# Kernel tuning notes

Measured on AMD Instinct MI355X. Metric: run time of the kernel, lower is better.

## Reference

```python
import jax, jax.numpy as jnp
import numpy as np

B, U, S, F, D = 4, 1024, 256, 16, 256
K_RED = 3          # fd_redundancy_k
MAX_STEPS = 32     # fixed trip count replacing the data-dependent while-loop
NEG = -1e9


def setup_inputs() -> dict:
    key = jax.random.key(0)
    ks = jax.random.split(key, 12)
    user_enc = jax.random.normal(ks[0], (B, U, D), dtype=jnp.float32)
    server_enc = jax.random.normal(ks[1], (B, S, D), dtype=jnp.float32)
    # small needs vs. generous capacities so the allocation loop runs many steps
    users = jax.random.uniform(ks[2], (B, U, 8), dtype=jnp.float32) * 0.1
    servers = jax.random.uniform(ks[3], (B, S, 8), dtype=jnp.float32) * 20.0 + 1.0
    connect = jax.random.uniform(ks[4], (B, U, S)) < 0.3
    fd_id = jax.random.randint(ks[5], (B, S), 0, F)
    fd_onehot = jax.nn.one_hot(fd_id, F, dtype=jnp.float32)
    W_state = jax.random.normal(ks[6], (D, 4), dtype=jnp.float32) * 0.5
    b_state = jnp.zeros((D,), dtype=jnp.float32)
    W_q = jax.random.normal(ks[7], (D, D), dtype=jnp.float32) * D ** -0.5
    W_k = jax.random.normal(ks[8], (D, D), dtype=jnp.float32) * D ** -0.5
    W_us = jax.random.normal(ks[9], (1, 3), dtype=jnp.float32) * 0.5
    return dict(user_enc=user_enc, server_enc=server_enc, users=users, servers=servers,
                connect=connect, fd_onehot=fd_onehot, W_state=W_state, b_state=b_state,
                W_q=W_q, W_k=W_k, W_us=W_us,
                fd_alpha=jnp.asarray(1.0, jnp.float32), fd_beta=jnp.asarray(0.0, jnp.float32),
                score_bias=jnp.asarray(0.0, jnp.float32))


def _forward(user_enc, server_enc, users, servers, connect, fd_onehot,
             W_state, b_state, W_q, W_k, W_us, fd_alpha, fd_beta, score_bias):
    b, u, _ = users.shape
    s = servers.shape[1]
    d = user_enc.shape[-1]
    needs = users[..., 2:6]            # [B,U,4]
    init_cap = servers[..., 3:7]       # [B,S,4]
    inv_sqrt_d = d ** -0.5
    kf = jnp.asarray(float(K_RED), jnp.float32)
    q = user_enc @ W_q.T               # [B,U,D]
    u_ids = jnp.arange(u)[None, :, None]   # [1,U,1]
    s_ids = jnp.arange(s)[None, None, :]   # [1,1,S]
    b_grid = jnp.broadcast_to(jnp.arange(b)[:, None], (b, s))

    def step(carry, _):
        cap, alloc, fd_seen, logp = carry
        rc = jnp.sum(alloc, axis=-1)                                   # [B,U]
        need_more = rc < K_RED
        can_fulfill = jnp.all(cap[:, None] >= needs[:, :, None], -1)   # [B,U,S]
        elig = connect & can_fulfill & need_more[:, :, None] & (~alloc)
        elig = elig & jnp.any(elig)                                    # freeze when done
        # fault-domain novelty score
        fd_overlap = jnp.einsum('buf,bsf->bus', fd_seen, fd_onehot)
        is_new_fd = (fd_overlap < 0.5).astype(jnp.float32)
        # capacity-conditioned server keys
        cap_ratio = cap / jnp.maximum(init_cap, 1e-6)
        k_vec = (server_enc + cap_ratio @ W_state.T + b_state) @ W_k.T
        logits = jnp.einsum('bud,bsd->bus', q, k_vec) * inv_sqrt_d + score_bias
        logits = logits + jnp.tanh(fd_alpha * is_new_fd + fd_beta)
        rc_f = rc.astype(jnp.float32)
        user_state = jnp.stack([rc_f / kf, jnp.clip(kf - rc_f, 0.0) / kf,
                                (rc == K_RED - 1).astype(jnp.float32)], axis=-1)
        logits = logits + user_state @ W_us.T                          # [B,U,1] bcast
        cand = jnp.where(elig, logits, NEG)
        valid_server = jnp.any(elig, axis=1)                           # [B,S]
        # each valid server proposes its best user (greedy policy)
        prop_u = jnp.argmax(cand, axis=1)                              # [B,S]
        logp_bs = jnp.max(cand, axis=1) - jax.scipy.special.logsumexp(cand, axis=1)
        prop_mask = valid_server[:, None, :] & (prop_u[:, None, :] == u_ids)  # [B,U,S]
        # each proposed user accepts its best proposing server
        chosen_s = jnp.argmax(jnp.where(prop_mask, logits, NEG), axis=-1)     # [B,U]
        has_prop = jnp.any(prop_mask, axis=-1)
        sel = has_prop[..., None] & (s_ids == chosen_s[..., None])     # [B,U,S]
        alloc = alloc | sel
        fd_contrib = jnp.where(valid_server[..., None], fd_onehot, 0.0)
        fd_seen = fd_seen.at[b_grid, prop_u].max(fd_contrib)
        used = jnp.einsum('bus,buc->bsc', sel.astype(jnp.float32), needs)
        cap = jnp.maximum(cap - used, 0.0)
        logp = logp + jnp.sum(jnp.where(prop_mask, logp_bs[:, None, :], 0.0), axis=-1)
        return (cap, alloc, fd_seen, logp), None

    init = (init_cap,
            jnp.zeros((b, u, s), dtype=bool),
            jnp.zeros((b, u, fd_onehot.shape[-1]), dtype=jnp.float32),
            jnp.zeros((b, u), dtype=jnp.float32))
    (cap, alloc, fd_seen, logp), _ = jax.lax.scan(step, init, None, length=MAX_STEPS)
    return logp.sum(axis=1), alloc, cap


def reference(user_enc, server_enc, users, servers, connect, fd_onehot,
              W_state, b_state, W_q, W_k, W_us, fd_alpha, fd_beta, score_bias):
    return _forward(user_enc, server_enc, users, servers, connect, fd_onehot,
                    W_state, b_state, W_q, W_k, W_us, fd_alpha, fd_beta, score_bias)
```

## Files before the change

kernel.cpp:

```cpp
#include <hip/hip_runtime.h>
#include <stdint.h>
#include <math.h>

#define NB 4
#define NU 1024
#define NS 256
#define NF 16
#define ND 256
#define NEGV -1000000000.0f
#define VBIT (1u << 14)
#define AGENT __HIP_MEMORY_SCOPE_AGENT
#define SPINCAP (1 << 20)
#define NGRP 64
#define SPB 4
#define NT 1024


__device__ __forceinline__ void gemm64_body(
    const float* __restrict__ A, const float* __restrict__ Bm, float* __restrict__ C,
    int K, int lda, int ldb, int ldc, const float* __restrict__ biasA, float alpha,
    int m0, int n0, int t,
    float (&As)[2][16][68], float (&Bs)[2][16][68]) {
  int tx = t & 15, ty = t >> 4;
  float acc[4][4];
#pragma unroll
  for (int i = 0; i < 4; i++)
#pragma unroll
    for (int j = 0; j < 4; j++) acc[i][j] = 0.f;
  int lr = t >> 2;
  int kq = (t & 3) * 4;
  {
    float4 av = *(const float4*)(A + (size_t)(m0 + lr) * lda + kq);
    if (biasA) {
      const float* bp = biasA + kq;
      av.x += bp[0]; av.y += bp[1]; av.z += bp[2]; av.w += bp[3];
    }
    As[0][kq + 0][lr] = av.x; As[0][kq + 1][lr] = av.y;
    As[0][kq + 2][lr] = av.z; As[0][kq + 3][lr] = av.w;
    float4 bv = *(const float4*)(Bm + (size_t)(n0 + lr) * ldb + kq);
    Bs[0][kq + 0][lr] = bv.x; Bs[0][kq + 1][lr] = bv.y;
    Bs[0][kq + 2][lr] = bv.z; Bs[0][kq + 3][lr] = bv.w;
  }
  __syncthreads();
  int nt = K >> 4;
  for (int ti = 0; ti < nt; ++ti) {
    int buf = ti & 1;
    float4 av2, bv2;
    bool more = (ti + 1 < nt);
    if (more) {
      int k0 = (ti + 1) << 4;
      av2 = *(const float4*)(A + (size_t)(m0 + lr) * lda + k0 + kq);
      if (biasA) {
        const float* bp = biasA + k0 + kq;
        av2.x += bp[0]; av2.y += bp[1]; av2.z += bp[2]; av2.w += bp[3];
      }
      bv2 = *(const float4*)(Bm + (size_t)(n0 + lr) * ldb + k0 + kq);
    }
#pragma unroll
    for (int k = 0; k < 16; ++k) {
      float4 a = *(const float4*)&As[buf][k][ty * 4];
      float4 bb = *(const float4*)&Bs[buf][k][tx * 4];
      float am[4] = {a.x, a.y, a.z, a.w};
      float bn[4] = {bb.x, bb.y, bb.z, bb.w};
#pragma unroll
      for (int i = 0; i < 4; ++i)
#pragma unroll
        for (int j = 0; j < 4; ++j) acc[i][j] += am[i] * bn[j];
    }
    if (more) {
      __syncthreads();
      int nb = buf ^ 1;
      As[nb][kq + 0][lr] = av2.x; As[nb][kq + 1][lr] = av2.y;
      As[nb][kq + 2][lr] = av2.z; As[nb][kq + 3][lr] = av2.w;
      Bs[nb][kq + 0][lr] = bv2.x; Bs[nb][kq + 1][lr] = bv2.y;
      Bs[nb][kq + 2][lr] = bv2.z; Bs[nb][kq + 3][lr] = bv2.w;
      __syncthreads();
    }
  }
#pragma unroll
  for (int i = 0; i < 4; ++i) {
    float4 o = make_float4(acc[i][0] * alpha, acc[i][1] * alpha,
                           acc[i][2] * alpha, acc[i][3] * alpha);
    *(float4*)(C + (size_t)(m0 + ty * 4 + i) * ldc + n0 + tx * 4) = o;
  }
}

__global__ __launch_bounds__(256) void k_pre1(
    const uint8_t* __restrict__ conn, const float* __restrict__ W_state,
    const float* __restrict__ W_k, const float* __restrict__ user_enc,
    const float* __restrict__ server_enc, const float* __restrict__ b_state,
    const float* __restrict__ W_q,
    uint32_t* __restrict__ connT, float* __restrict__ WS_K,
    float* __restrict__ q, float* __restrict__ kb, float4* __restrict__ propZ) {
  __shared__ float As[2][16][68];
  __shared__ float Bs[2][16][68];
  int blk = blockIdx.x;
  int t = threadIdx.x;
  if (blk < 128) {
    __shared__ unsigned dd[2];
    unsigned c0 = 0, c123 = 0;
    for (int i = t; i < 4096; i += 256) {
      uchar4 v = ((const uchar4*)conn)[i];
      c0 |= v.x; c123 |= (unsigned)(v.y | v.z | v.w);
    }
    if (t == 0) { dd[0] = 0; dd[1] = 0; }
    __syncthreads();
    unsigned long long m0 = __ballot(c0 != 0), m1 = __ballot(c123 != 0);
    if ((t & 63) == 0) {
      if (m0) atomicOr(&dd[0], 1u);
      if (m1) atomicOr(&dd[1], 1u);
    }
    __syncthreads();
    int f = (dd[1] == 0) ? 0 : ((dd[0] == 0) ? 1 : 2);
    int b = blk >> 5, ug = blk & 31;
    int u0 = ug * 32;
    uint8_t* sm = (uint8_t*)&As[0][0][0];
#pragma unroll 4
    for (int r = 0; r < 32; ++r) {
      int e = (b * NU + u0 + r) * NS + t;
      bool nz;
      if (f == 0)      nz = ((const int*)conn)[e] != 0;
      else if (f == 1) nz = ((const float*)conn)[e] != 0.0f;
      else             nz = conn[e] != 0;
      sm[r * 260 + t] = nz ? 1 : 0;
    }
    __syncthreads();
    uint32_t word = 0;
#pragma unroll
    for (int j = 0; j < 32; ++j) word |= (uint32_t)sm[j * 260 + t] << j;
    connT[(b * NS + t) * 32 + ug] = word;
  } else if (blk == 128) {
    int d = t;
    const float4* wk4 = (const float4*)(W_k + d * ND);
    const float4* ws4 = (const float4*)W_state;
    float a0 = 0, a1 = 0, a2 = 0, a3 = 0;
    for (int e4 = 0; e4 < ND / 4; ++e4) {
      float4 k4 = wk4[e4];
      float4 w0 = ws4[e4 * 4 + 0];
      a0 += k4.x * w0.x; a1 += k4.x * w0.y; a2 += k4.x * w0.z; a3 += k4.x * w0.w;
      float4 w1 = ws4[e4 * 4 + 1];
      a0 += k4.y * w1.x; a1 += k4.y * w1.y; a2 += k4.y * w1.z; a3 += k4.y * w1.w;
      float4 w2 = ws4[e4 * 4 + 2];
      a0 += k4.z * w2.x; a1 += k4.z * w2.y; a2 += k4.z * w2.z; a3 += k4.z * w2.w;
      float4 w3 = ws4[e4 * 4 + 3];
      a0 += k4.w * w3.x; a1 += k4.w * w3.y; a2 += k4.w * w3.z; a3 += k4.w * w3.w;
    }
    ((float4*)WS_K)[d] = make_float4(a0, a1, a2, a3);
  } else if (blk < 385) {
    int idx = blk - 129;
    gemm64_body(user_enc, W_q, q, ND, ND, ND, ND, nullptr, 1.f,
                (idx >> 2) * 64, (idx & 3) * 64, t, As, Bs);
  } else if (blk < 449) {
    int idx = blk - 385;
    gemm64_body(server_enc, W_k, kb, ND, ND, ND, ND, b_state, 1.f,
                (idx >> 2) * 64, (idx & 3) * 64, t, As, Bs);
  } else {
    float4 z = make_float4(0.f, 0.f, 0.f, 0.f);
    for (int i = t; i < 2048; i += 256) propZ[i] = z;
  }
}

__global__ __launch_bounds__(256) void k_pre2(const float* __restrict__ q,
                                              const float* __restrict__ WS_K,
                                              float* __restrict__ qc,
                                              const float* __restrict__ kb,
                                              float* __restrict__ L0T) {
  __shared__ float As[2][16][68];
  __shared__ float Bs[2][16][68];
  int blk = blockIdx.x;
  int t = threadIdx.x;
  if (blk < 1024) {
    int row = blk * 4 + (t >> 6);
    int ln = t & 63;
    const float* qr = q + (size_t)row * ND;
    float a0 = 0, a1 = 0, a2 = 0, a3 = 0;
    for (int d = ln; d < ND; d += 64) {
      float qv = qr[d];
      float4 w = ((const float4*)WS_K)[d];
      a0 += qv * w.x; a1 += qv * w.y; a2 += qv * w.z; a3 += qv * w.w;
    }
    for (int o = 32; o; o >>= 1) {
      a0 += __shfl_xor(a0, o); a1 += __shfl_xor(a1, o);
      a2 += __shfl_xor(a2, o); a3 += __shfl_xor(a3, o);
    }
    if (ln == 0)
      ((float4*)qc)[row] = make_float4(a0 * 0.0625f, a1 * 0.0625f, a2 * 0.0625f, a3 * 0.0625f);
  } else {
    int idx = blk - 1024;
    int z = idx >> 6;
    int rest = idx & 63;
    int m0 = (rest >> 4) * 64;
    int n0 = (rest & 15) * 64;
    gemm64_body(kb + (size_t)z * NS * ND, q + (size_t)z * NU * ND,
                L0T + (size_t)z * NS * NU, ND, ND, ND, NU, nullptr, 0.0625f,
                m0, n0, t, As, Bs);
  }
}

__global__ __launch_bounds__(NT) void k_steps4(
    const float* __restrict__ L0T, const float* __restrict__ qc,
    const float* __restrict__ users, const float* __restrict__ servers,
    const uint32_t* __restrict__ connT, const float* __restrict__ fd_onehot,
    const float* __restrict__ W_us, const float* __restrict__ fd_alpha,
    const float* __restrict__ fd_beta, const float* __restrict__ score_bias,
    unsigned long long* __restrict__ propA, unsigned long long* __restrict__ propB,
    float* __restrict__ out) {
  __shared__ float redM[SPB][NT];
  __shared__ int redA[SPB][NT];
  __shared__ unsigned keyEnc4[4][NU];
  __shared__ unsigned srvMin4[4][NU];
  __shared__ float lsum4[4][NU];
  __shared__ unsigned fdSh4[4][NU];
  __shared__ float4 capS4[SPB];
  __shared__ float4 crS4[SPB];
  __shared__ float4 minv4[SPB];
  __shared__ int fidS[SPB];
  __shared__ float pM[SPB][4];
  __shared__ int pA[SPB][4];
  __shared__ float pS[SPB][4];
  __shared__ float bM[SPB];
  __shared__ float wredL[16];
  __shared__ int anyL[4];

  const int blk = blockIdx.x;
  const int b = (blk & 7) >> 1;
  const int g = ((blk >> 3) << 1) | (blk & 1);
  const int tid = threadIdx.x;
  const int wv = tid >> 6, ln64 = tid & 63;
  const int bs0 = b * NS + g * SPB;
  const int bank = tid & 3;
  const int sW = wv >> 2, part = wv & 3;

  const float a_ = fd_alpha[0], be_ = fd_beta[0];
  const float t0 = tanhf(be_), t1 = tanhf(a_ + be_);
  const float sb = score_bias[0];
  const float w0 = W_us[0], w1 = W_us[1], w2 = W_us[2];

  if (tid < SPB) {
    int srow = bs0 + tid;
    int f = 0;
    for (int ff = 0; ff < NF; ++ff)
      if (fd_onehot[srow * NF + ff] > 0.5f) { f = ff; break; }
    fidS[tid] = f;
    float4 ic = make_float4(servers[srow * 8 + 3], servers[srow * 8 + 4],
                            servers[srow * 8 + 5], servers[srow * 8 + 6]);
    capS4[tid] = ic;
    float4 mv = make_float4(fmaxf(ic.x, 1e-6f), fmaxf(ic.y, 1e-6f),
                            fmaxf(ic.z, 1e-6f), fmaxf(ic.w, 1e-6f));
    minv4[tid] = mv;
    crS4[tid] = make_float4(ic.x / mv.x, ic.y / mv.y, ic.z / mv.z, ic.w / mv.w);
  }

  const int gu = b * NU + tid;
  float4 q4 = *(const float4*)(qc + gu * 4);
  float2 nA = *(const float2*)(users + gu * 8 + 2);
  float2 nB2 = *(const float2*)(users + gu * 8 + 4);
  const float nax = nA.x, nay = nA.y, nbx = nB2.x, nby = nB2.y;
  float L0r[SPB];
  uint32_t upk = 0;
  float usv = w1;
  float logpv = 0.f;
  uint32_t cb = 0, ab = 0;
#pragma unroll
  for (int s = 0; s < SPB; ++s) {
    L0r[s] = L0T[(size_t)(bs0 + s) * NU + tid];
    uint32_t word = connT[(bs0 + s) * 32 + (tid >> 5)];
    cb |= ((word >> (tid & 31)) & 1u) << s;
  }
  for (int i = tid; i < 4 * NU; i += NT) {
    (&keyEnc4[0][0])[i] = 0u;
    (&srvMin4[0][0])[i] = 0xFFFFFFFFu;
    (&lsum4[0][0])[i] = 0.f;
    (&fdSh4[0][0])[i] = 0u;
  }
  __syncthreads();

  for (int step = 0; step < 32; ++step) {
    unsigned e = (unsigned)(step + 1);
    float cand[SPB];
#pragma unroll
    for (int s = 0; s < SPB; ++s) {
      float4 c = capS4[s];
      float4 cr = crS4[s];
      int fid = fidS[s];
      bool el = ((cb >> s) & 1u) && !((ab >> s) & 1u) &&
                ((upk & 0x30000u) != 0x30000u) &&
                c.x >= nax && c.y >= nay && c.z >= nbx && c.w >= nby;
      float tt = ((upk >> fid) & 1u) ? t0 : t1;
      float lg = L0r[s] + q4.x * cr.x + q4.y * cr.y + q4.z * cr.z + q4.w * cr.w +
                 sb + tt + usv;
      float cv = el ? lg : NEGV;
      cand[s] = cv;
      redM[s][tid] = cv;
      redA[s][tid] = (cv > NEGV) ? tid : 0x7fffffff;
    }
    __syncthreads();
    {
      int base = part * 256 + ln64 * 4;
      float m = redM[sW][base]; int a = redA[sW][base];
#pragma unroll
      for (int j = 1; j < 4; ++j) {
        float v = redM[sW][base + j]; int aa = redA[sW][base + j];
        if (v > m || (v == m && aa < a)) { m = v; a = aa; }
      }
      for (int o = 32; o; o >>= 1) {
        float ov = __shfl_xor(m, o); int oa = __shfl_xor(a, o);
        if (ov > m || (ov == m && oa < a)) { m = ov; a = oa; }
      }
      if (ln64 == 0) { pM[sW][part] = m; pA[sW][part] = a; }
    }
    __syncthreads();
    if (tid < SPB) {
      float m = pM[tid][0]; int a = pA[tid][0];
#pragma unroll
      for (int j = 1; j < 4; ++j) {
        float v = pM[tid][j]; int aa = pA[tid][j];
        if (v > m || (v == m && aa < a)) { m = v; a = aa; }
      }
      bM[tid] = m;
      int au = (a == 0x7fffffff) ? 0 : a;
      unsigned validb = (m > -1e8f) ? VBIT : 0u;
      unsigned pinfo = (unsigned)au | ((unsigned)fidS[tid] << 10) | validb | (e << 15);
      unsigned long long Aw = (unsigned long long)pinfo |
                              ((unsigned long long)__float_as_uint(m) << 32);
      __hip_atomic_store(&propA[(step & 1) * (NB * NS) + bs0 + tid], Aw,
                         __ATOMIC_RELAXED, AGENT);
    }
    __syncthreads();
#pragma unroll
    for (int s = 0; s < SPB; ++s)
      redM[s][tid] = expf(cand[s] - bM[s]);
    __syncthreads();
    {
      int base = part * 256 + ln64 * 4;
      float ps = redM[sW][base] + redM[sW][base + 1] + redM[sW][base + 2] +
                 redM[sW][base + 3];
      for (int o = 32; o; o >>= 1) ps += __shfl_xor(ps, o);
      if (ln64 == 0) pS[sW][part] = ps;
    }
    __syncthreads();
    if (tid < SPB) {
      float ps = pS[tid][0] + pS[tid][1] + pS[tid][2] + pS[tid][3];
      unsigned long long Bw = (unsigned long long)__float_as_uint(-logf(ps)) |
                              ((unsigned long long)e << 32);
      __hip_atomic_store(&propB[(step & 1) * (NB * NS) + bs0 + tid], Bw,
                         __ATOMIC_RELAXED, AGENT);
    }

    {
      int par = (step & 1) * (NB * NS) + b * NS;
      unsigned pi = 0;
      unsigned encv = 0;
      int pu = 0;
      if (tid < 256) {
        unsigned long long Aw = __hip_atomic_load(&propA[par + tid], __ATOMIC_RELAXED, AGENT);
        if ((((unsigned)Aw >> 15) & 63u) != e) {
          int iters = 0;
          do {
            __builtin_amdgcn_s_sleep(1);
            Aw = __hip_atomic_load(&propA[par + tid], __ATOMIC_RELAXED, AGENT);
            if (++iters > SPINCAP) break;
          } while ((((unsigned)Aw >> 15) & 63u) != e);
        }
        pi = (unsigned)Aw;
        pu = pi & 1023;
        if (pi & VBIT) {
          unsigned vb = (unsigned)(Aw >> 32);
          encv = (vb & 0x80000000u) ? ~vb : (vb | 0x80000000u);
          atomicMax(&keyEnc4[bank][pu], encv);
        }
      }
      unsigned long long mm = __ballot((pi & VBIT) != 0);
      if (wv < 4 && ln64 == 0) anyL[wv] = (mm != 0ull) ? 1 : 0;
      __syncthreads();
      if (!(anyL[0] | anyL[1] | anyL[2] | anyL[3])) break;
      if ((tid < 256) && (pi & VBIT)) {
        if (keyEnc4[bank][pu] == encv)
          atomicMin(&srvMin4[bank][pu], (unsigned)tid);
        unsigned long long Bw = __hip_atomic_load(&propB[par + tid], __ATOMIC_RELAXED, AGENT);
        if ((unsigned)(Bw >> 32) != e) {
          int iters = 0;
          do {
            __builtin_amdgcn_s_sleep(1);
            Bw = __hip_atomic_load(&propB[par + tid], __ATOMIC_RELAXED, AGENT);
            if (++iters > SPINCAP) break;
          } while ((unsigned)(Bw >> 32) != e);
        }
        atomicAdd(&lsum4[bank][pu], __uint_as_float((unsigned)Bw));
        atomicOr(&fdSh4[bank][pu], 1u << ((pi >> 10) & 15));
      }
      __syncthreads();
      {
        int u = tid;
        unsigned k0 = keyEnc4[0][u], k1 = keyEnc4[1][u];
        unsigned k2 = keyEnc4[2][u], k3 = keyEnc4[3][u];
        unsigned gmax = max(max(k0, k1), max(k2, k3));
        if (gmax) {
          unsigned win = 0xFFFFFFFFu;
          if (k0 == gmax) win = min(win, srvMin4[0][u]);
          if (k1 == gmax) win = min(win, srvMin4[1][u]);
          if (k2 == gmax) win = min(win, srvMin4[2][u]);
          if (k3 == gmax) win = min(win, srvMin4[3][u]);
          float ls = lsum4[0][u] + lsum4[1][u] + lsum4[2][u] + lsum4[3][u];
          unsigned fda = fdSh4[0][u] | fdSh4[1][u] | fdSh4[2][u] | fdSh4[3][u];
          keyEnc4[0][u] = 0u; keyEnc4[1][u] = 0u; keyEnc4[2][u] = 0u; keyEnc4[3][u] = 0u;
          srvMin4[0][u] = 0xFFFFFFFFu; srvMin4[1][u] = 0xFFFFFFFFu;
          srvMin4[2][u] = 0xFFFFFFFFu; srvMin4[3][u] = 0xFFFFFFFFu;
          lsum4[0][u] = 0.f; lsum4[1][u] = 0.f; lsum4[2][u] = 0.f; lsum4[3][u] = 0.f;
          fdSh4[0][u] = 0u; fdSh4[1][u] = 0u; fdSh4[2][u] = 0u; fdSh4[3][u] = 0u;
          logpv += ls;
          uint32_t pk = upk;
          int r = (int)((pk >> 16) & 3) + 1;
          upk = ((pk | fda) & 0xFFFFu) | ((uint32_t)r << 16);
          float rf = (float)r;
          usv = w0 * (rf / 3.0f) + w1 * (fmaxf(3.0f - rf, 0.f) / 3.0f) +
                ((r == 2) ? w2 : 0.f);
          if ((int)(win >> 2) == g) {
            int sl = win & 3;
            ab |= 1u << sl;
            float4 c = capS4[sl];
            float4 nc = make_float4(fmaxf(c.x - nax, 0.f), fmaxf(c.y - nay, 0.f),
                                    fmaxf(c.z - nbx, 0.f), fmaxf(c.w - nby, 0.f));
            capS4[sl] = nc;
            float4 mv = minv4[sl];
            crS4[sl] = make_float4(nc.x / mv.x, nc.y / mv.y, nc.z / mv.z, nc.w / mv.w);
          }
        }
      }
      __syncthreads();
    }
  }

  {
    float4 o;
    o.x = (ab & 1u) ? 1.f : 0.f;
    o.y = ((ab >> 1) & 1u) ? 1.f : 0.f;
    o.z = ((ab >> 2) & 1u) ? 1.f : 0.f;
    o.w = ((ab >> 3) & 1u) ? 1.f : 0.f;
    *(float4*)(out + 4 + (size_t)(b * NU + tid) * NS + g * 4) = o;
  }
  if (tid < SPB)
    *(float4*)(out + 4 + (size_t)NB * NU * NS + (size_t)(bs0 + tid) * 4) = capS4[tid];
  if (g == 0) {
    float a2 = logpv;
    for (int o = 32; o; o >>= 1) a2 += __shfl_xor(a2, o);
    if (ln64 == 0) wredL[wv] = a2;
    __syncthreads();
    if (tid == 0) {
      float s = 0.f;
#pragma unroll
      for (int i = 0; i < 16; ++i) s += wredL[i];
      out[b] = s;
    }
  }
}

extern "C" void kernel_launch(void* const* d_in, const int* in_sizes, int n_in,
                              void* d_out, int out_size, void* d_ws, size_t ws_size,
                              hipStream_t stream) {
  const float* user_enc = (const float*)d_in[0];
  const float* server_enc = (const float*)d_in[1];
  const float* users = (const float*)d_in[2];
  const float* servers = (const float*)d_in[3];
  const uint8_t* connect = (const uint8_t*)d_in[4];
  const float* fd_onehot = (const float*)d_in[5];
  const float* W_state = (const float*)d_in[6];
  const float* b_state = (const float*)d_in[7];
  const float* W_q = (const float*)d_in[8];
  const float* W_k = (const float*)d_in[9];
  const float* W_us = (const float*)d_in[10];
  const float* fd_alpha = (const float*)d_in[11];
  const float* fd_beta = (const float*)d_in[12];
  const float* score_bias = (const float*)d_in[13];

  char* ws = (char*)d_ws;
  size_t off = 0;
  auto take = [&](size_t bytes) -> void* {
    size_t cur = off;
    off = (off + bytes + 255) & ~(size_t)255;
    return (void*)(ws + cur);
  };
  unsigned long long* propA = (unsigned long long*)take((size_t)2 * NB * NS * 8);
  unsigned long long* propB = (unsigned long long*)take((size_t)2 * NB * NS * 8);
  float* q = (float*)take((size_t)NB * NU * ND * 4);
  float* kb = (float*)take((size_t)NB * NS * ND * 4);
  float* L0T = (float*)take((size_t)NB * NS * NU * 4);
  float* qc = (float*)take((size_t)NB * NU * 4 * 4);
  float* WS_K = (float*)take((size_t)ND * 4 * 4);
  uint32_t* connT = (uint32_t*)take((size_t)NB * NS * 32 * 4);
  float* outp = (float*)d_out;

  k_pre1<<<450, 256, 0, stream>>>(connect, W_state, W_k, user_enc, server_enc, b_state,
                                  W_q, connT, WS_K, q, kb, (float4*)propA);
  k_pre2<<<1280, 256, 0, stream>>>(q, WS_K, qc, kb, L0T);
  k_steps4<<<NB * NGRP, NT, 0, stream>>>(
      L0T, qc, users, servers, connT, fd_onehot, W_us, fd_alpha, fd_beta, score_bias,
      propA, propB, outp);
}
```

Before: 184.7 us.

## Defer log-sum consumption one step and fuse max broadcast into exp-sum

Every wave now finishes the per-server max reduction redundantly, which removes the single-thread bM broadcast and two block barriers. The exp is computed directly inside the sum reduction instead of going through a shared-memory round trip. Waiting on propB, the normaliser published by other blocks, is moved one step later, so cross-block latency overlaps the next step's work instead of stalling the current step. Risk: lsum accumulation is deferred, so logp and the lsum reset must stay consistent. Stale lsum state in the per-step consume/reset logic could be double-counted or lost, and the final tail flush does not spin-wait.

```diff
diff --git a/kernel.cpp b/kernel.cpp
--- a/kernel.cpp
+++ b/kernel.cpp
@@ -218,7 +218,6 @@
   __shared__ float pM[SPB][4];
   __shared__ int pA[SPB][4];
   __shared__ float pS[SPB][4];
-  __shared__ float bM[SPB];
   __shared__ float wredL[16];
   __shared__ int anyL[4];
 
@@ -261,6 +260,8 @@
   float usv = w1;
   float logpv = 0.f;
   uint32_t cb = 0, ab = 0;
+  int prevPu = 0, prevSlot = 0;
+  bool prevValid = false;
 #pragma unroll
   for (int s = 0; s < SPB; ++s) {
     L0r[s] = L0T[(size_t)(bs0 + s) * NU + tid];
@@ -310,31 +311,27 @@
       if (ln64 == 0) { pM[sW][part] = m; pA[sW][part] = a; }
     }
     __syncthreads();
-    if (tid < SPB) {
-      float m = pM[tid][0]; int a = pA[tid][0];
+    float bm;
+    {
+      float m = pM[sW][0]; int a = pA[sW][0];
 #pragma unroll
       for (int j = 1; j < 4; ++j) {
-        float v = pM[tid][j]; int aa = pA[tid][j];
+        float v = pM[sW][j]; int aa = pA[sW][j];
         if (v > m || (v == m && aa < a)) { m = v; a = aa; }
       }
-      bM[tid] = m;
-      int au = (a == 0x7fffffff) ? 0 : a;
-      unsigned validb = (m > -1e8f) ? VBIT : 0u;
-      unsigned pinfo = (unsigned)au | ((unsigned)fidS[tid] << 10) | validb | (e << 15);
-      unsigned long long Aw = (unsigned long long)pinfo |
-                              ((unsigned long long)__float_as_uint(m) << 32);
-      __hip_atomic_store(&propA[(step & 1) * (NB * NS) + bs0 + tid], Aw,
-                         __ATOMIC_RELAXED, AGENT);
-    }
-    __syncthreads();
-#pragma unroll
-    for (int s = 0; s < SPB; ++s)
-      redM[s][tid] = expf(cand[s] - bM[s]);
-    __syncthreads();
-    {
+      bm = m;
+      if (part == 0 && ln64 == 0) {
+        int au = (a == 0x7fffffff) ? 0 : a;
+        unsigned validb = (m > -1e8f) ? VBIT : 0u;
+        unsigned pinfo = (unsigned)au | ((unsigned)fidS[sW] << 10) | validb | (e << 15);
+        unsigned long long Aw = (unsigned long long)pinfo |
+                                ((unsigned long long)__float_as_uint(m) << 32);
+        __hip_atomic_store(&propA[(step & 1) * (NB * NS) + bs0 + sW], Aw,
+                           __ATOMIC_RELAXED, AGENT);
+      }
       int base = part * 256 + ln64 * 4;
-      float ps = redM[sW][base] + redM[sW][base + 1] + redM[sW][base + 2] +
-                 redM[sW][base + 3];
+      float ps = expf(redM[sW][base] - bm) + expf(redM[sW][base + 1] - bm) +
+                 expf(redM[sW][base + 2] - bm) + expf(redM[sW][base + 3] - bm);
       for (int o = 32; o; o >>= 1) ps += __shfl_xor(ps, o);
       if (ln64 == 0) pS[sW][part] = ps;
     }
@@ -364,6 +361,21 @@
         }
         pi = (unsigned)Aw;
         pu = pi & 1023;
+        if (prevValid) {
+          unsigned long long Bw = __hip_atomic_load(&propB[prevSlot], __ATOMIC_RELAXED, AGENT);
+          if ((unsigned)(Bw >> 32) != (unsigned)step) {
+            int iters = 0;
+            do {
+              __builtin_amdgcn_s_sleep(1);
+              Bw = __hip_atomic_load(&propB[prevSlot], __ATOMIC_RELAXED, AGENT);
+              if (++iters > SPINCAP) break;
+            } while ((unsigned)(Bw >> 32) != (unsigned)step);
+          }
+          atomicAdd(&lsum4[bank][prevPu], __uint_as_float((unsigned)Bw));
+        }
+        prevValid = (pi & VBIT) != 0;
+        prevPu = pu;
+        prevSlot = par + tid;
         if (pi & VBIT) {
           unsigned vb = (unsigned)(Aw >> 32);
           encv = (vb & 0x80000000u) ? ~vb : (vb | 0x80000000u);
@@ -377,16 +389,6 @@
       if ((tid < 256) && (pi & VBIT)) {
         if (keyEnc4[bank][pu] == encv)
           atomicMin(&srvMin4[bank][pu], (unsigned)tid);
-        unsigned long long Bw = __hip_atomic_load(&propB[par + tid], __ATOMIC_RELAXED, AGENT);
-        if ((unsigned)(Bw >> 32) != e) {
-          int iters = 0;
-          do {
-            __builtin_amdgcn_s_sleep(1);
-            Bw = __hip_atomic_load(&propB[par + tid], __ATOMIC_RELAXED, AGENT);
-            if (++iters > SPINCAP) break;
-          } while ((unsigned)(Bw >> 32) != e);
-        }
-        atomicAdd(&lsum4[bank][pu], __uint_as_float((unsigned)Bw));
         atomicOr(&fdSh4[bank][pu], 1u << ((pi >> 10) & 15));
       }
       __syncthreads();
@@ -431,6 +433,13 @@
     }
   }
 
+  if ((tid < 256) && prevValid) {
+    unsigned long long Bw = __hip_atomic_load(&propB[prevSlot], __ATOMIC_RELAXED, AGENT);
+    atomicAdd(&lsum4[bank][prevPu], __uint_as_float((unsigned)Bw));
+  }
+  __syncthreads();
+  logpv += lsum4[0][tid] + lsum4[1][tid] + lsum4[2][tid] + lsum4[3][tid];
+
   {
     float4 o;
     o.x = (ab & 1u) ? 1.f : 0.f;
```

After: 177.4 us. 4.0% less time.
